# Kernel optimization log

Hardware: AMD Instinct MI355X
Metric: run time of the kernel (lower is better)

## Reference

```python
import jax, jax.numpy as jnp
import numpy as np

D_IN = 1024
D_OUT = 1024
NUM_HEADS = 16
HEAD_DIM = D_OUT // NUM_HEADS


def setup_inputs() -> dict:
    key = jax.random.key(0)
    ks = jax.random.split(key, 6)
    s = 0.02
    x = jax.random.normal(ks[0], (1, 4096, D_IN), dtype=jnp.float32)
    W_q = jax.random.normal(ks[1], (D_IN, D_OUT), dtype=jnp.float32) * s
    W_k = jax.random.normal(ks[2], (D_IN, D_OUT), dtype=jnp.float32) * s
    W_v = jax.random.normal(ks[3], (D_IN, D_OUT), dtype=jnp.float32) * s
    W_o = jax.random.normal(ks[4], (D_OUT, D_OUT), dtype=jnp.float32) * s
    b_o = jnp.zeros((D_OUT,), dtype=jnp.float32)
    return {"x": x, "W_q": W_q, "W_k": W_k, "W_v": W_v, "W_o": W_o, "b_o": b_o}


def reference(x, W_q, W_k, W_v, W_o, b_o):
    b, n, _ = x.shape
    # project and split heads: [b, h, n, d]
    def split_heads(t):
        return t.reshape(b, n, NUM_HEADS, HEAD_DIM).transpose(0, 2, 1, 3)
    q = split_heads(x @ W_q)
    k = split_heads(x @ W_k)
    v = split_heads(x @ W_v)
    scale = 1.0 / jnp.sqrt(jnp.float32(HEAD_DIM))
    scores = jnp.einsum('bhqd,bhkd->bhqk', q, k) * scale  # [b,h,n,n]
    causal = jnp.tril(jnp.ones((n, n), dtype=bool))
    scores = jnp.where(causal, scores, -jnp.inf)
    weights = jax.nn.softmax(scores, axis=-1)
    # dropout rate is 0.0 -> identity
    ctx = jnp.einsum('bhqk,bhkd->bhqd', weights, v)
    ctx = ctx.transpose(0, 2, 1, 3).reshape(b, n, D_OUT)
    return ctx @ W_o + b_o
```

## Files before the change

kernel.cpp:

```cpp
#include <hip/hip_runtime.h>
#include <hip/hip_bf16.h>

typedef __hip_bfloat16 bf16;
typedef __attribute__((ext_vector_type(8))) short short8;
typedef __attribute__((ext_vector_type(4))) float floatx4;

#define SEQ 4096
#define DIM 1024
#define NH 16
#define HD 64

__device__ __forceinline__ short f2s(float f) { bf16 t = __float2bfloat16(f); return *(short*)&t; }

__device__ __forceinline__ void gload16(const void* g, void* l) {
    __builtin_amdgcn_global_load_lds(
        (const __attribute__((address_space(1))) void*)g,
        (__attribute__((address_space(3))) void*)l, 16, 0, 0);
}

__device__ __forceinline__ short8 cvt8(float4 a, float4 b) {
    short8 s;
    s[0] = f2s(a.x); s[1] = f2s(a.y); s[2] = f2s(a.z); s[3] = f2s(a.w);
    s[4] = f2s(b.x); s[5] = f2s(b.y); s[6] = f2s(b.z); s[7] = f2s(b.w);
    return s;
}

__global__ __launch_bounds__(256) void transpose_cast_kernel(
    const float* __restrict__ W0, const float* __restrict__ W1,
    const float* __restrict__ W2, const float* __restrict__ W3,
    bf16* __restrict__ Wt_all)
{
    const float* W = blockIdx.z == 0 ? W0 : blockIdx.z == 1 ? W1
                   : blockIdx.z == 2 ? W2 : W3;
    bf16* Wt = Wt_all + (size_t)blockIdx.z * DIM * DIM;

    __shared__ float tile[32][33];
    const int n0 = blockIdx.x * 32, k0 = blockIdx.y * 32;
    const int tr = threadIdx.x >> 5;
    const int tc = threadIdx.x & 31;
#pragma unroll
    for (int i = 0; i < 32; i += 8)
        tile[tr + i][tc] = W[(size_t)(k0 + tr + i) * DIM + n0 + tc];
    __syncthreads();
#pragma unroll
    for (int i = 0; i < 32; i += 8)
        Wt[(size_t)(n0 + tr + i) * DIM + k0 + tc] = __float2bfloat16(tile[tc][tr + i]);
}

#define QBM 128
#define QBN 128
#define QBK 64

__global__ __launch_bounds__(256) void qkv_gemm_kernel(
    const float* __restrict__ A, const bf16* __restrict__ Wt,
    bf16* __restrict__ Qb, bf16* __restrict__ Kb, bf16* __restrict__ Vb)
{
    const int z = blockIdx.z;
    const bf16* Bt = Wt + (size_t)z * DIM * DIM;
    bf16* C = z == 0 ? Qb : (z == 1 ? Kb : Vb);
    const float osc = (z == 0) ? 0.125f : 1.0f;

    __shared__ alignas(16) float Af[QBM][QBK];
    __shared__ alignas(16) short Bs[QBN][QBK];

    const int tid  = threadIdx.x;
    const int wave = tid >> 6, lane = tid & 63;
    const int l15  = lane & 15, quad = lane >> 4;
    const int wm = (wave & 1) * 64;
    const int wn = (wave >> 1) * 64;
    const int bm = blockIdx.y * QBM;
    const int bn = blockIdx.x * QBN;

    const int arow = tid >> 4;
    const int agch = (tid & 15) ^ (arow & 15);
    const float* gA = A + (size_t)(bm + arow) * DIM + agch * 4;
    char* ldsA = (char*)&Af[0][0] + wave * 1024;

    const int brow = tid >> 3;
    const int bgch = (tid & 7) ^ (brow & 7);
    const bf16* gB = Bt + (size_t)(bn + brow) * DIM + bgch * 8;
    char* ldsB = (char*)&Bs[0][0] + wave * 1024;

    floatx4 acc[4][4] = {};

    for (int k0 = 0; k0 < DIM; k0 += QBK) {
        __syncthreads();
#pragma unroll
        for (int c = 0; c < 8; ++c)
            gload16(gA + (size_t)c * 16 * DIM + k0, ldsA + c * 4096);
#pragma unroll
        for (int c = 0; c < 4; ++c)
            gload16(gB + (size_t)c * 32 * DIM + k0, ldsB + c * 4096);
        __syncthreads();

#pragma unroll
        for (int c2 = 0; c2 < 2; ++c2) {
            const int g0 = c2 * 8 + quad * 2;
            const int cb = (c2 * 4 + quad) ^ (l15 & 7);
            short8 afr[4], bfr[4];
#pragma unroll
            for (int i = 0; i < 4; ++i) {
                const int ra = wm + i * 16 + l15;
                float4 f0 = *(const float4*)&Af[ra][(g0 ^ l15) * 4];
                float4 f1 = *(const float4*)&Af[ra][((g0 + 1) ^ l15) * 4];
                afr[i] = cvt8(f0, f1);
                bfr[i] = *(const short8*)&Bs[wn + i * 16 + l15][cb * 8];
            }
#pragma unroll
            for (int mi = 0; mi < 4; ++mi)
#pragma unroll
                for (int ni = 0; ni < 4; ++ni)
                    acc[mi][ni] = __builtin_amdgcn_mfma_f32_16x16x32_bf16(
                        afr[mi], bfr[ni], acc[mi][ni], 0, 0, 0);
        }
    }

#pragma unroll
    for (int mi = 0; mi < 4; ++mi)
#pragma unroll
        for (int r = 0; r < 4; ++r) {
            const int row = bm + wm + mi * 16 + quad * 4 + r;
#pragma unroll
            for (int ni = 0; ni < 4; ++ni) {
                const int col = bn + wn + ni * 16 + l15;
                C[(size_t)row * DIM + col] = __float2bfloat16(acc[mi][ni][r] * osc);
            }
        }
}

__global__ __launch_bounds__(256) void out_gemm_kernel(
    const bf16* __restrict__ A, const bf16* __restrict__ Bt,
    const float* __restrict__ bias, float* __restrict__ C)
{
    __shared__ alignas(16) short Asl[128][64];
    __shared__ alignas(16) short Bsl[64][64];

    const int tid  = threadIdx.x;
    const int wave = tid >> 6, lane = tid & 63;
    const int l15  = lane & 15, quad = lane >> 4;
    const int wm = (wave & 1) * 64;
    const int wn = (wave >> 1) * 32;
    const int bm = blockIdx.y * 128;
    const int bn = blockIdx.x * 64;

    const int srow   = tid >> 3;
    const int gchunk = (tid & 7) ^ (srow & 7);
    const bf16* gA = A  + (size_t)(bm + srow) * DIM + gchunk * 8;
    const bf16* gB = Bt + (size_t)(bn + srow) * DIM + gchunk * 8;
    char* ldsA = (char*)&Asl[0][0] + wave * 1024;
    char* ldsB = (char*)&Bsl[0][0] + wave * 1024;

    floatx4 acc[4][2] = {};

    for (int k0 = 0; k0 < DIM; k0 += 64) {
        __syncthreads();
#pragma unroll
        for (int c = 0; c < 4; ++c)
            gload16(gA + (size_t)c * 32 * DIM + k0, ldsA + c * 4096);
#pragma unroll
        for (int c = 0; c < 2; ++c)
            gload16(gB + (size_t)c * 32 * DIM + k0, ldsB + c * 4096);
        __syncthreads();

#pragma unroll
        for (int c2 = 0; c2 < 2; ++c2) {
            const int cb = (c2 * 4 + quad) ^ (l15 & 7);
            short8 afr[4], bfr[2];
#pragma unroll
            for (int i = 0; i < 4; ++i)
                afr[i] = *(const short8*)&Asl[wm + i * 16 + l15][cb * 8];
#pragma unroll
            for (int i = 0; i < 2; ++i)
                bfr[i] = *(const short8*)&Bsl[wn + i * 16 + l15][cb * 8];
#pragma unroll
            for (int mi = 0; mi < 4; ++mi)
#pragma unroll
                for (int ni = 0; ni < 2; ++ni)
                    acc[mi][ni] = __builtin_amdgcn_mfma_f32_16x16x32_bf16(
                        afr[mi], bfr[ni], acc[mi][ni], 0, 0, 0);
        }
    }

#pragma unroll
    for (int mi = 0; mi < 4; ++mi)
#pragma unroll
        for (int r = 0; r < 4; ++r) {
            const int row = bm + wm + mi * 16 + quad * 4 + r;
#pragma unroll
            for (int ni = 0; ni < 2; ++ni) {
                const int col = bn + wn + ni * 16 + l15;
                C[(size_t)row * DIM + col] = acc[mi][ni][r] + bias[col];
            }
        }
}

#define QT 128
#define KT 64
#define LDT 72

__global__ __launch_bounds__(256) void flash_attn_kernel(
    const bf16* __restrict__ Q, const bf16* __restrict__ K,
    const bf16* __restrict__ V, bf16* ctx)
{
    const int lin  = blockIdx.y * 32 + blockIdx.x;
    const int half = lin >> 8, idx = lin & 255;
    const int qj   = half ? (idx & 31) : 31 - (idx & 31);
    const int h    = (idx >> 5) + 8 * half;
    const int q0   = qj * QT;
    const int nkt  = 2 * qj + 2;

    const int tid  = threadIdx.x;
    const int wave = tid >> 6;
    const int lane = tid & 63;
    const int l15  = lane & 15;
    const int quad = lane >> 4;

    __shared__ alignas(16) short Qs[QT][LDT];
    __shared__ alignas(16) short Ks[KT][LDT];
    __shared__ alignas(16) short Vt[HD][LDT];
    __shared__ alignas(16) short Ps[4][2][16][LDT];

    {
        const int r = tid >> 1, cb = (tid & 1) * 32;
        const short8* src = (const short8*)(Q + (size_t)(q0 + r) * DIM + h * HD + cb);
#pragma unroll
        for (int i = 0; i < 4; ++i)
            *(short8*)&Qs[r][cb + 8 * i] = src[i];
    }

    const int kr = tid >> 2, kc = (tid & 3) * 16;
    const int vr = (tid & 31) * 2, vd = (tid >> 5) * 8;

    short8 kreg0, kreg1, vreg0, vreg1;
    {
        const short8* kp  = (const short8*)(K + (size_t)kr * DIM + h * HD + kc);
        kreg0 = kp[0]; kreg1 = kp[1];
        const short8* vp0 = (const short8*)(V + (size_t)vr * DIM + h * HD + vd);
        const short8* vp1 = (const short8*)(V + (size_t)(vr + 1) * DIM + h * HD + vd);
        vreg0 = vp0[0]; vreg1 = vp1[0];
    }

    __syncthreads();
    short8 qfrag[2][2];
#pragma unroll
    for (int s = 0; s < 2; ++s)
#pragma unroll
        for (int c = 0; c < 2; ++c)
            qfrag[s][c] = *(const short8*)&Qs[wave * 32 + s * 16 + l15][c * 32 + quad * 8];

    short8 onesf;
#pragma unroll
    for (int i = 0; i < 8; ++i) onesf[i] = (short)0x3F80;

    floatx4 o_acc[2][4] = {};
    floatx4 lacc[2] = {};

    for (int kt = 0; kt < nkt; ++kt) {
        __syncthreads();

        *(short8*)&Ks[kr][kc]     = kreg0;
        *(short8*)&Ks[kr][kc + 8] = kreg1;
#pragma unroll
        for (int i = 0; i < 8; ++i) {
            unsigned int pv = (unsigned int)(unsigned short)vreg0[i]
                            | ((unsigned int)(unsigned short)vreg1[i] << 16);
            *(unsigned int*)&Vt[vd + i][vr] = pv;
        }
        if (kt + 1 < nkt) {
            const size_t nb = (size_t)(kt + 1) * KT;
            const short8* kp  = (const short8*)(K + (nb + kr) * DIM + h * HD + kc);
            kreg0 = kp[0]; kreg1 = kp[1];
            const short8* vp0 = (const short8*)(V + (nb + vr) * DIM + h * HD + vd);
            const short8* vp1 = (const short8*)(V + (nb + vr + 1) * DIM + h * HD + vd);
            vreg0 = vp0[0]; vreg1 = vp1[0];
        }
        __syncthreads();

        floatx4 s_acc[2][4] = {};
#pragma unroll
        for (int n = 0; n < 4; ++n)
#pragma unroll
            for (int c = 0; c < 2; ++c) {
                short8 kf = *(const short8*)&Ks[n * 16 + l15][c * 32 + quad * 8];
#pragma unroll
                for (int s = 0; s < 2; ++s)
                    s_acc[s][n] = __builtin_amdgcn_mfma_f32_16x16x32_bf16(
                        qfrag[s][c], kf, s_acc[s][n], 0, 0, 0);
            }

        const int kbase = kt * KT;
        const bool diag = (kt >= nkt - 2);
        if (diag) {
#pragma unroll
            for (int s = 0; s < 2; ++s)
#pragma unroll
                for (int n = 0; n < 4; ++n)
#pragma unroll
                    for (int r = 0; r < 4; ++r) {
                        const int key  = kbase + n * 16 + l15;
                        const int qrow = q0 + wave * 32 + s * 16 + quad * 4 + r;
                        float p = (key <= qrow) ? __expf(s_acc[s][n][r]) : 0.f;
                        Ps[wave][s][quad * 4 + r][n * 16 + l15] = f2s(p);
                    }
        } else {
#pragma unroll
            for (int s = 0; s < 2; ++s)
#pragma unroll
                for (int n = 0; n < 4; ++n)
#pragma unroll
                    for (int r = 0; r < 4; ++r)
                        Ps[wave][s][quad * 4 + r][n * 16 + l15] = f2s(__expf(s_acc[s][n][r]));
        }

        short8 pfrag[2][2];
#pragma unroll
        for (int s = 0; s < 2; ++s) {
            pfrag[s][0] = *(const short8*)&Ps[wave][s][l15][quad * 8];
            pfrag[s][1] = *(const short8*)&Ps[wave][s][l15][32 + quad * 8];
        }
#pragma unroll
        for (int n = 0; n < 4; ++n)
#pragma unroll
            for (int c = 0; c < 2; ++c) {
                short8 vf = *(const short8*)&Vt[n * 16 + l15][c * 32 + quad * 8];
#pragma unroll
                for (int s = 0; s < 2; ++s)
                    o_acc[s][n] = __builtin_amdgcn_mfma_f32_16x16x32_bf16(
                        pfrag[s][c], vf, o_acc[s][n], 0, 0, 0);
            }
#pragma unroll
        for (int s = 0; s < 2; ++s) {
            lacc[s] = __builtin_amdgcn_mfma_f32_16x16x32_bf16(pfrag[s][0], onesf, lacc[s], 0, 0, 0);
            lacc[s] = __builtin_amdgcn_mfma_f32_16x16x32_bf16(pfrag[s][1], onesf, lacc[s], 0, 0, 0);
        }
    }

#pragma unroll
    for (int s = 0; s < 2; ++s)
#pragma unroll
        for (int r = 0; r < 4; ++r) {
            const float inv = 1.0f / lacc[s][r];
            const int row = q0 + wave * 32 + s * 16 + quad * 4 + r;
#pragma unroll
            for (int n = 0; n < 4; ++n)
                ctx[(size_t)row * DIM + h * HD + n * 16 + l15] =
                    __float2bfloat16(o_acc[s][n][r] * inv);
        }
}

extern "C" void kernel_launch(void* const* d_in, const int* in_sizes, int n_in,
                              void* d_out, int out_size, void* d_ws, size_t ws_size,
                              hipStream_t stream)
{
    const float* x  = (const float*)d_in[0];
    const float* Wq = (const float*)d_in[1];
    const float* Wk = (const float*)d_in[2];
    const float* Wv = (const float*)d_in[3];
    const float* Wo = (const float*)d_in[4];
    const float* bo = (const float*)d_in[5];
    float* out = (float*)d_out;

    bf16* Wt_all = (bf16*)d_ws;
    bf16* Qb     = Wt_all + (size_t)4 * DIM * DIM;
    bf16* V      = (bf16*)d_out;
    bf16* Kb     = V + (size_t)SEQ * DIM;
    bf16* ctx    = Qb;
    const bf16* Wot = Wt_all + (size_t)3 * DIM * DIM;

    transpose_cast_kernel<<<dim3(32, 32, 4), 256, 0, stream>>>(Wq, Wk, Wv, Wo, Wt_all);

    qkv_gemm_kernel<<<dim3(DIM / QBN, SEQ / QBM, 3), 256, 0, stream>>>(
        x, Wt_all, Qb, Kb, V);

    flash_attn_kernel<<<dim3(32, NH), 256, 0, stream>>>(Qb, Kb, V, ctx);

    out_gemm_kernel<<<dim3(DIM / 64, SEQ / 128), 256, 0, stream>>>(
        ctx, Wot, bo, out);
}
```

Baseline: 211.5 us.

## Double-buffer K/V shared tiles and transpose QK MFMA for vectorized P stores

K and V^T tiles in shared memory become double-buffered. The next tile is written to the alternate buffer after the current tile's MFMAs, which cuts one of the two barriers per iteration and hides register-to-LDS staging behind compute. The QK^T MFMA operands are swapped so each lane holds four consecutive keys for one query row. That lets P be written to LDS as packed 4-element stores instead of scalar shorts. The cost is double the K/V shared memory, which may reduce occupancy.

```diff
diff --git a/kernel.cpp b/kernel.cpp
--- a/kernel.cpp
+++ b/kernel.cpp
@@ -3,6 +3,7 @@
 
 typedef __hip_bfloat16 bf16;
 typedef __attribute__((ext_vector_type(8))) short short8;
+typedef __attribute__((ext_vector_type(4))) short short4v;
 typedef __attribute__((ext_vector_type(4))) float floatx4;
 
 #define SEQ 4096
@@ -216,8 +217,8 @@
     const int quad = lane >> 4;
 
     __shared__ alignas(16) short Qs[QT][LDT];
-    __shared__ alignas(16) short Ks[KT][LDT];
-    __shared__ alignas(16) short Vt[HD][LDT];
+    __shared__ alignas(16) short Ks[2][KT][LDT];
+    __shared__ alignas(16) short Vt[2][HD][LDT];
     __shared__ alignas(16) short Ps[4][2][16][LDT];
 
     {
@@ -239,8 +240,25 @@
         const short8* vp1 = (const short8*)(V + (size_t)(vr + 1) * DIM + h * HD + vd);
         vreg0 = vp0[0]; vreg1 = vp1[0];
     }
+    *(short8*)&Ks[0][kr][kc]     = kreg0;
+    *(short8*)&Ks[0][kr][kc + 8] = kreg1;
+#pragma unroll
+    for (int i = 0; i < 8; ++i) {
+        unsigned int pv = (unsigned int)(unsigned short)vreg0[i]
+                        | ((unsigned int)(unsigned short)vreg1[i] << 16);
+        *(unsigned int*)&Vt[0][vd + i][vr] = pv;
+    }
+    {
+        const size_t nb = (size_t)KT;
+        const short8* kp  = (const short8*)(K + (nb + kr) * DIM + h * HD + kc);
+        kreg0 = kp[0]; kreg1 = kp[1];
+        const short8* vp0 = (const short8*)(V + (nb + vr) * DIM + h * HD + vd);
+        const short8* vp1 = (const short8*)(V + (nb + vr + 1) * DIM + h * HD + vd);
+        vreg0 = vp0[0]; vreg1 = vp1[0];
+    }
 
     __syncthreads();
+
     short8 qfrag[2][2];
 #pragma unroll
     for (int s = 0; s < 2; ++s)
@@ -256,60 +274,48 @@
     floatx4 lacc[2] = {};
 
     for (int kt = 0; kt < nkt; ++kt) {
-        __syncthreads();
-
-        *(short8*)&Ks[kr][kc]     = kreg0;
-        *(short8*)&Ks[kr][kc + 8] = kreg1;
-#pragma unroll
-        for (int i = 0; i < 8; ++i) {
-            unsigned int pv = (unsigned int)(unsigned short)vreg0[i]
-                            | ((unsigned int)(unsigned short)vreg1[i] << 16);
-            *(unsigned int*)&Vt[vd + i][vr] = pv;
-        }
-        if (kt + 1 < nkt) {
-            const size_t nb = (size_t)(kt + 1) * KT;
-            const short8* kp  = (const short8*)(K + (nb + kr) * DIM + h * HD + kc);
-            kreg0 = kp[0]; kreg1 = kp[1];
-            const short8* vp0 = (const short8*)(V + (nb + vr) * DIM + h * HD + vd);
-            const short8* vp1 = (const short8*)(V + (nb + vr + 1) * DIM + h * HD + vd);
-            vreg0 = vp0[0]; vreg1 = vp1[0];
-        }
-        __syncthreads();
-
-        floatx4 s_acc[2][4] = {};
+        const int b = kt & 1;
+
+        floatx4 sT[2][4] = {};
 #pragma unroll
         for (int n = 0; n < 4; ++n)
 #pragma unroll
             for (int c = 0; c < 2; ++c) {
-                short8 kf = *(const short8*)&Ks[n * 16 + l15][c * 32 + quad * 8];
+                short8 kf = *(const short8*)&Ks[b][n * 16 + l15][c * 32 + quad * 8];
 #pragma unroll
                 for (int s = 0; s < 2; ++s)
-                    s_acc[s][n] = __builtin_amdgcn_mfma_f32_16x16x32_bf16(
-                        qfrag[s][c], kf, s_acc[s][n], 0, 0, 0);
+                    sT[s][n] = __builtin_amdgcn_mfma_f32_16x16x32_bf16(
+                        kf, qfrag[s][c], sT[s][n], 0, 0, 0);
             }
 
         const int kbase = kt * KT;
-        const bool diag = (kt >= nkt - 2);
-        if (diag) {
+        if (kt >= nkt - 2) {
+#pragma unroll
+            for (int s = 0; s < 2; ++s) {
+                const int qrow = q0 + wave * 32 + s * 16 + l15;
+#pragma unroll
+                for (int n = 0; n < 4; ++n) {
+                    const int key0 = kbase + n * 16 + quad * 4;
+                    short4v pk;
+#pragma unroll
+                    for (int r = 0; r < 4; ++r) {
+                        float p = (key0 + r <= qrow) ? __expf(sT[s][n][r]) : 0.f;
+                        pk[r] = f2s(p);
+                    }
+                    *(short4v*)&Ps[wave][s][l15][n * 16 + quad * 4] = pk;
+                }
+            }
+        } else {
 #pragma unroll
             for (int s = 0; s < 2; ++s)
 #pragma unroll
-                for (int n = 0; n < 4; ++n)
-#pragma unroll
-                    for (int r = 0; r < 4; ++r) {
-                        const int key  = kbase + n * 16 + l15;
-                        const int qrow = q0 + wave * 32 + s * 16 + quad * 4 + r;
-                        float p = (key <= qrow) ? __expf(s_acc[s][n][r]) : 0.f;
-                        Ps[wave][s][quad * 4 + r][n * 16 + l15] = f2s(p);
-                    }
-        } else {
-#pragma unroll
-            for (int s = 0; s < 2; ++s)
-#pragma unroll
-                for (int n = 0; n < 4; ++n)
+                for (int n = 0; n < 4; ++n) {
+                    short4v pk;
 #pragma unroll
                     for (int r = 0; r < 4; ++r)
-                        Ps[wave][s][quad * 4 + r][n * 16 + l15] = f2s(__expf(s_acc[s][n][r]));
+                        pk[r] = f2s(__expf(sT[s][n][r]));
+                    *(short4v*)&Ps[wave][s][l15][n * 16 + quad * 4] = pk;
+                }
         }
 
         short8 pfrag[2][2];
@@ -322,7 +328,7 @@
         for (int n = 0; n < 4; ++n)
 #pragma unroll
             for (int c = 0; c < 2; ++c) {
-                short8 vf = *(const short8*)&Vt[n * 16 + l15][c * 32 + quad * 8];
+                short8 vf = *(const short8*)&Vt[b][n * 16 + l15][c * 32 + quad * 8];
 #pragma unroll
                 for (int s = 0; s < 2; ++s)
                     o_acc[s][n] = __builtin_amdgcn_mfma_f32_16x16x32_bf16(
@@ -333,6 +339,26 @@
             lacc[s] = __builtin_amdgcn_mfma_f32_16x16x32_bf16(pfrag[s][0], onesf, lacc[s], 0, 0, 0);
             lacc[s] = __builtin_amdgcn_mfma_f32_16x16x32_bf16(pfrag[s][1], onesf, lacc[s], 0, 0, 0);
         }
+
+        if (kt + 1 < nkt) {
+            *(short8*)&Ks[b ^ 1][kr][kc]     = kreg0;
+            *(short8*)&Ks[b ^ 1][kr][kc + 8] = kreg1;
+#pragma unroll
+            for (int i = 0; i < 8; ++i) {
+                unsigned int pv = (unsigned int)(unsigned short)vreg0[i]
+                                | ((unsigned int)(unsigned short)vreg1[i] << 16);
+                *(unsigned int*)&Vt[b ^ 1][vd + i][vr] = pv;
+            }
+            if (kt + 2 < nkt) {
+                const size_t nb = (size_t)(kt + 2) * KT;
+                const short8* kp  = (const short8*)(K + (nb + kr) * DIM + h * HD + kc);
+                kreg0 = kp[0]; kreg1 = kp[1];
+                const short8* vp0 = (const short8*)(V + (nb + vr) * DIM + h * HD + vd);
+                const short8* vp1 = (const short8*)(V + (nb + vr + 1) * DIM + h * HD + vd);
+                vreg0 = vp0[0]; vreg1 = vp1[0];
+            }
+        }
+        __syncthreads();
     }
 
 #pragma unroll
```

Result: faster. 198.3 us (-6.3%).
